# Kernel optimization log

Hardware: AMD Instinct MI355X
Metric: run time of the kernel (lower is better)

## Reference

```python
import jax, jax.numpy as jnp
import numpy as np

K = 20          # neighbors per point
BN_EPS = 1e-5


def setup_inputs() -> dict:
    key = jax.random.key(0)
    k0, k1, k2 = jax.random.split(key, 3)
    B, N, C_OUT, EDGE_DIM = 8, 4096, 64, 4  # edge feat = [diff(3), ||diff||(1)]
    x = jax.random.normal(k0, (B, N, 3), dtype=jnp.float32)
    pos = jax.random.uniform(k1, (B, N, 3), dtype=jnp.float32)
    # shared 1x1-conv MLP params (Conv1d k=1 == per-edge linear) + BatchNorm affine
    W = jax.random.normal(k2, (C_OUT, EDGE_DIM), dtype=jnp.float32) * 0.1
    b = jnp.zeros((C_OUT,), jnp.float32)
    gamma = jnp.ones((C_OUT,), jnp.float32)
    beta = jnp.zeros((C_OUT,), jnp.float32)
    return {"x": x, "pos": pos, "W": W, "b": b, "gamma": gamma, "beta": beta}


def _knn_idx(pos, k):
    # pos: [B, N, 3] -> idx of k nearest neighbors per point, self excluded. [B, N, k]
    B, N, _ = pos.shape
    sq = jnp.sum(pos * pos, axis=-1)                                   # [B, N]
    d2 = sq[:, :, None] + sq[:, None, :] - 2.0 * jnp.einsum('bnd,bmd->bnm', pos, pos)
    d2 = d2 + jnp.eye(N, dtype=pos.dtype) * 1e10                       # exclude self-loop
    _, idx = jax.lax.top_k(-d2, k)                                     # [B, N, k]
    return idx


def _forward(pos, W, b, gamma, beta, k=K):
    idx = _knn_idx(pos, k)                                             # [B, N, k] (int, non-diff)
    nbr = jax.vmap(lambda p, i: p[i])(pos, idx)                        # gather: [B, N, k, 3]
    diff = nbr - pos[:, :, None, :]                                    # neighbor - center
    dist = jnp.sqrt(jnp.sum(diff * diff, axis=-1, keepdims=True))      # [B, N, k, 1]
    feat = jnp.concatenate([diff, dist], axis=-1)                      # [B, N, k, 4]
    # shared MLP (1x1 conv): per-edge linear
    y = jnp.einsum('bnkc,oc->bnko', feat, W) + b                       # [B, N, k, 64]
    # BatchNorm1d over all edges (training-mode batch stats), per channel
    mu = jnp.mean(y, axis=(0, 1, 2))
    var = jnp.var(y, axis=(0, 1, 2))
    y = (y - mu) * jax.lax.rsqrt(var + BN_EPS) * gamma + beta
    y = jax.nn.relu(y)
    y = jnp.where(y >= 0, y, 0.1 * y)   # leaky_relu(0.1) from source (no-op after relu, kept for fidelity)
    return jnp.mean(y, axis=2)          # mean pool over each node's k edges -> [B, N, 64]


def reference(x, pos, W, b, gamma, beta):
    # x only provides (batch_size, num_points) in the source; math uses pos.
    return _forward(pos, W, b, gamma, beta)
```

## Files before the change

### kernel.cpp

```cpp
#include <hip/hip_runtime.h>

#define NB    8
#define NP    4096
#define KNN   20
#define COUT  64
#define S     4
#define BLK   256
#define QPB   (BLK / S)
#define BPB   (NP / QPB)
#define NBLK1 (NB * BPB)
#define NBLK2 ((NB * NP * 4) / BLK)
#define NMOM  14
#define MSTR  16
#define LCAP  32
#define FBIG  3.402823466e38f

typedef unsigned long long u64;
typedef unsigned int u32;

__device__ __forceinline__ void ins20(float d, u32 mi,
                                      float* __restrict__ bd,
                                      u32* __restrict__ bi) {
#pragma unroll
    for (int j = KNN - 1; j >= 1; --j) {
        const bool sh  = d < bd[j - 1];
        const bool in_ = !sh && (d < bd[j]);
        bi[j] = sh ? bi[j - 1] : (in_ ? mi : bi[j]);
        bd[j] = fminf(fmaxf(bd[j - 1], d), bd[j]);
    }
    if (d < bd[0]) { bi[0] = mi; bd[0] = d; }
}

__global__ __launch_bounds__(BLK, 2)
void knn_kernel(const float* __restrict__ pos,
                unsigned short* __restrict__ idx_out,
                float* __restrict__ mom) {
    __shared__ float4 sp[NP];

    const int b = blockIdx.x / BPB;
    const int t = threadIdx.x;
    const int s = t & (S - 1);
    const int n = (blockIdx.x % BPB) * QPB + (t >> 2);
    const float* pb = pos + (size_t)b * NP * 3;

    for (int i = t; i < NP; i += BLK) {
        const float x = pb[3 * i], y = pb[3 * i + 1], z = pb[3 * i + 2];
        const float csq = __fadd_rn(
            __fadd_rn(__fmul_rn(x, x), __fmul_rn(y, y)), __fmul_rn(z, z));
        sp[i] = make_float4(x, y, z, csq);
    }
    __syncthreads();

    const float4 q = sp[n];

    float sd0 = FBIG, sd1 = FBIG, sd2 = FBIG, sd3 = FBIG, sd4 = FBIG;
#pragma unroll 4
    for (int i = 0; i < NP / S; i += 4) {
        const int m = (i << 2) | s;
        const float4 c = sp[m];
        const float dot = fmaf(q.z, c.z, fmaf(q.y, c.y, __fmul_rn(q.x, c.x)));
        const float d2  = __fsub_rn(__fadd_rn(q.w, c.w), __fmul_rn(2.0f, dot));
        if (m != n && d2 < sd4) {
            sd4 = fminf(fmaxf(sd3, d2), sd4);
            sd3 = fminf(fmaxf(sd2, d2), sd3);
            sd2 = fminf(fmaxf(sd1, d2), sd2);
            sd1 = fminf(fmaxf(sd0, d2), sd1);
            sd0 = fminf(sd0, d2);
        }
    }
    float gb = sd4;
    gb = fmaxf(gb, __shfl_xor(gb, 1));
    gb = fmaxf(gb, __shfl_xor(gb, 2));

    float bd[KNN];
    u32   bi[KNN];
#pragma unroll
    for (int j = 0; j < KNN; ++j) { bd[j] = FBIG; bi[j] = 0xFFFu; }
    float p0d = 0.f, p1d = 0.f, p2d = 0.f, p3d = 0.f;
    u32   p0i = 0, p1i = 0, p2i = 0, p3i = 0;
    int   cnt = 0;

#pragma unroll 2
    for (int i = 0; i < NP / S; ++i) {
        const int m = (i << 2) | s;
        const float4 c = sp[m];
        const float dot = fmaf(q.z, c.z, fmaf(q.y, c.y, __fmul_rn(q.x, c.x)));
        const float d2  = __fsub_rn(__fadd_rn(q.w, c.w), __fmul_rn(2.0f, dot));
        const bool acc = (m != n) && (d2 <= gb);
        const bool a0 = acc && (cnt == 0), a1 = acc && (cnt == 1);
        const bool a2 = acc && (cnt == 2), a3 = acc && (cnt == 3);
        p0d = a0 ? d2 : p0d;  p0i = a0 ? (u32)m : p0i;
        p1d = a1 ? d2 : p1d;  p1i = a1 ? (u32)m : p1i;
        p2d = a2 ? d2 : p2d;  p2i = a2 ? (u32)m : p2i;
        p3d = a3 ? d2 : p3d;  p3i = a3 ? (u32)m : p3i;
        cnt += (int)acc;
        if (__ballot(cnt == 4)) {
            ins20(cnt >= 1 ? p0d : FBIG, p0i, bd, bi);
            ins20(cnt >= 2 ? p1d : FBIG, p1i, bd, bi);
            ins20(cnt >= 3 ? p2d : FBIG, p2i, bd, bi);
            ins20(cnt >= 4 ? p3d : FBIG, p3i, bd, bi);
            cnt = 0;
            float g = bd[KNN - 1];
            g = fminf(g, __shfl_xor(g, 1));
            g = fminf(g, __shfl_xor(g, 2));
            gb = fminf(gb, g);
        }
    }
    ins20(cnt >= 1 ? p0d : FBIG, p0i, bd, bi);
    ins20(cnt >= 2 ? p1d : FBIG, p1i, bd, bi);
    ins20(cnt >= 3 ? p2d : FBIG, p2i, bd, bi);
    ins20(cnt >= 4 ? p3d : FBIG, p3i, bd, bi);

    u64 key[LCAP];
#pragma unroll
    for (int j = 0; j < KNN; ++j) {
        u32 fb = __float_as_uint(bd[j]);
        fb ^= (u32)((int)fb >> 31) | 0x80000000u;
        key[j] = ((u64)fb << 12) | bi[j];
    }
#pragma unroll
    for (int j = KNN; j < LCAP; ++j) key[j] = ~0ull;

#pragma unroll
    for (int r = 1; r <= 2; r <<= 1) {
#pragma unroll
        for (int j = 0; j < LCAP / 2; ++j) {
            const int k2 = LCAP - 1 - j;
            const u64 pa = (u64)__shfl_xor((long long)key[k2], r);
            const u64 pc = (u64)__shfl_xor((long long)key[j],  r);
            key[j]  = key[j]  < pa ? key[j]  : pa;
            key[k2] = key[k2] < pc ? key[k2] : pc;
        }
#pragma unroll
        for (int d = 16; d >= 1; d >>= 1) {
#pragma unroll
            for (int j = 0; j < LCAP; ++j) {
                if ((j & d) == 0) {
                    const u64 x = key[j], y = key[j + d];
                    key[j]     = x < y ? x : y;
                    key[j + d] = x < y ? y : x;
                }
            }
        }
    }

    unsigned short* ip = idx_out + ((size_t)b * NP + n) * KNN;
    float s1x = 0, s1y = 0, s1z = 0, s1d = 0;
    float mxx = 0, mxy = 0, mxz = 0, mxd = 0;
    float myy = 0, myz = 0, myd = 0;
    float mzz = 0, mzd = 0, mdd = 0;
#pragma unroll
    for (int j = 0; j < KNN; ++j) {
        const int m = (int)(key[j] & 0xFFFull);
        if ((j & 3) == s) ip[j] = (unsigned short)m;
        const float4 c = sp[m];
        const float dx = __fsub_rn(c.x, q.x);
        const float dy = __fsub_rn(c.y, q.y);
        const float dz = __fsub_rn(c.z, q.z);
        const float dd = sqrtf(__fadd_rn(
            __fadd_rn(__fmul_rn(dx, dx), __fmul_rn(dy, dy)), __fmul_rn(dz, dz)));
        s1x += dx; s1y += dy; s1z += dz; s1d += dd;
        mxx += dx * dx; mxy += dx * dy; mxz += dx * dz; mxd += dx * dd;
        myy += dy * dy; myz += dy * dz; myd += dy * dd;
        mzz += dz * dz; mzd += dz * dd; mdd += dd * dd;
    }
    {
        float vals[NMOM] = {s1x, s1y, s1z, s1d,
                            mxx, mxy, mxz, mxd, myy, myz, myd, mzz, mzd, mdd};
#pragma unroll
        for (int tt = 0; tt < NMOM; ++tt) {
            float v = vals[tt];
#pragma unroll
            for (int off = 32; off > 0; off >>= 1) v += __shfl_down(v, off);
            if ((t & 63) == 0) atomicAdd(&mom[tt * MSTR], v * 0.25f);
        }
    }
}

__global__ __launch_bounds__(BLK)
void out_kernel(const float* __restrict__ pos,
                const float* __restrict__ W,
                const float* __restrict__ bias,
                const float* __restrict__ gamma,
                const float* __restrict__ beta,
                const unsigned short* __restrict__ idx_in,
                const float* __restrict__ mom,
                float* __restrict__ out) {
    __shared__ float sWp[COUT][4];
    __shared__ float sbp[COUT];

    if (threadIdx.x < COUT) {
        const int o = threadIdx.x;
        double S1[4], s2v[10];
#pragma unroll
        for (int tt = 0; tt < 4; ++tt)  S1[tt]  = (double)mom[tt * MSTR];
#pragma unroll
        for (int tt = 0; tt < 10; ++tt) s2v[tt] = (double)mom[(4 + tt) * MSTR];
        const double M = (double)NB * NP * KNN;
        double mean[4];
#pragma unroll
        for (int c = 0; c < 4; ++c) mean[c] = S1[c] / M;
        double E2[4][4];
        E2[0][0] = s2v[0]; E2[0][1] = E2[1][0] = s2v[1];
        E2[0][2] = E2[2][0] = s2v[2]; E2[0][3] = E2[3][0] = s2v[3];
        E2[1][1] = s2v[4]; E2[1][2] = E2[2][1] = s2v[5];
        E2[1][3] = E2[3][1] = s2v[6];
        E2[2][2] = s2v[7]; E2[2][3] = E2[3][2] = s2v[8];
        E2[3][3] = s2v[9];
        double w[4];
#pragma unroll
        for (int c = 0; c < 4; ++c) w[c] = (double)W[o * 4 + c];
        const double bo = (double)bias[o];
        double mu = bo;
#pragma unroll
        for (int c = 0; c < 4; ++c) mu += w[c] * mean[c];
        double var = 0.0;
#pragma unroll
        for (int c = 0; c < 4; ++c)
#pragma unroll
            for (int c2 = 0; c2 < 4; ++c2)
                var += w[c] * w[c2] * (E2[c][c2] / M - mean[c] * mean[c2]);
        const double scale = (double)gamma[o] / sqrt(var + 1e-5);
#pragma unroll
        for (int c = 0; c < 4; ++c) sWp[o][c] = (float)(w[c] * scale);
        sbp[o] = (float)((bo - mu) * scale + (double)beta[o]);
    }
    __syncthreads();

    const int t  = threadIdx.x;
    const int gq = blockIdx.x * (BLK / 4) + (t >> 2);
    const int b  = gq / NP, n = gq % NP;
    const int c0 = (t & 3) * 16;
    const float* pb = pos + (size_t)b * NP * 3;
    const float qx = pb[3 * n], qy = pb[3 * n + 1], qz = pb[3 * n + 2];

    float fx[KNN], fy[KNN], fz[KNN], fd[KNN];
    const unsigned short* ip = idx_in + (size_t)gq * KNN;
#pragma unroll
    for (int j = 0; j < KNN; ++j) {
        const int m = ip[j];
        const float dx = __fsub_rn(pb[3 * m], qx);
        const float dy = __fsub_rn(pb[3 * m + 1], qy);
        const float dz = __fsub_rn(pb[3 * m + 2], qz);
        fx[j] = dx; fy[j] = dy; fz[j] = dz;
        fd[j] = sqrtf(__fadd_rn(
            __fadd_rn(__fmul_rn(dx, dx), __fmul_rn(dy, dy)), __fmul_rn(dz, dz)));
    }

    float* ob = out + (size_t)gq * COUT + c0;
    const float inv = 1.0f / (float)KNN;
#pragma unroll
    for (int o = 0; o < 16; o += 4) {
        float acc[4];
#pragma unroll
        for (int qq = 0; qq < 4; ++qq) {
            const float w0 = sWp[c0 + o + qq][0], w1 = sWp[c0 + o + qq][1];
            const float w2 = sWp[c0 + o + qq][2], w3 = sWp[c0 + o + qq][3];
            const float bb = sbp[c0 + o + qq];
            float a = 0.f;
#pragma unroll
            for (int j = 0; j < KNN; ++j) {
                float y = fmaf(fx[j], w0,
                          fmaf(fy[j], w1, fmaf(fz[j], w2, fmaf(fd[j], w3, bb))));
                a += fmaxf(y, 0.f);
            }
            acc[qq] = a * inv;
        }
        float4 p = {acc[0], acc[1], acc[2], acc[3]};
        *reinterpret_cast<float4*>(ob + o) = p;
    }
}

extern "C" void kernel_launch(void* const* d_in, const int* in_sizes, int n_in,
                              void* d_out, int out_size, void* d_ws, size_t ws_size,
                              hipStream_t stream) {
    (void)in_sizes; (void)n_in; (void)out_size; (void)ws_size;
    const float* pos   = (const float*)d_in[1];
    const float* W     = (const float*)d_in[2];
    const float* bias  = (const float*)d_in[3];
    const float* gamma = (const float*)d_in[4];
    const float* beta  = (const float*)d_in[5];
    float* out = (float*)d_out;

    float* mom = (float*)d_ws;
    unsigned short* idxws = (unsigned short*)((char*)d_ws + 1024);

    hipMemsetAsync(mom, 0, NMOM * MSTR * sizeof(float), stream);
    knn_kernel<<<NBLK1, BLK, 0, stream>>>(pos, idxws, mom);
    out_kernel<<<NBLK2, BLK, 0, stream>>>(pos, W, bias, gamma, beta,
                                          idxws, mom, out);
}
```

Measured before the change: 295.9 us.

## Materialize edge features in kNN kernel to skip gather in output kernel

The kNN kernel now writes each edge's (dx,dy,dz,dist) as a float4 into workspace, and a new output kernel reads those features contiguously instead of gathering neighbor positions by index and recomputing differences and sqrt. This removes scattered position loads in the second kernel but adds a write and a read of about 10 MB of edge features (8*4096*20*16 bytes). It falls back to the old path when the workspace is too small.

```diff
diff --git a/kernel.cpp b/kernel.cpp
--- a/kernel.cpp
+++ b/kernel.cpp
@@ -34,6 +34,7 @@
 __global__ __launch_bounds__(BLK, 2)
 void knn_kernel(const float* __restrict__ pos,
                 unsigned short* __restrict__ idx_out,
+                float4* __restrict__ feats,
                 float* __restrict__ mom) {
     __shared__ float4 sp[NP];
 
@@ -159,6 +160,8 @@
         const float dz = __fsub_rn(c.z, q.z);
         const float dd = sqrtf(__fadd_rn(
             __fadd_rn(__fmul_rn(dx, dx), __fmul_rn(dy, dy)), __fmul_rn(dz, dz)));
+        if (feats != nullptr && (j & 3) == s)
+            feats[((size_t)b * NP + n) * KNN + j] = make_float4(dx, dy, dz, dd);
         s1x += dx; s1y += dy; s1z += dz; s1d += dd;
         mxx += dx * dx; mxy += dx * dy; mxz += dx * dz; mxd += dx * dd;
         myy += dy * dy; myz += dy * dz; myd += dy * dd;
@@ -174,6 +177,99 @@
             for (int off = 32; off > 0; off >>= 1) v += __shfl_down(v, off);
             if ((t & 63) == 0) atomicAdd(&mom[tt * MSTR], v * 0.25f);
         }
+    }
+}
+
+__device__ __forceinline__ void bn_fold(const float* __restrict__ W,
+                                        const float* __restrict__ bias,
+                                        const float* __restrict__ gamma,
+                                        const float* __restrict__ beta,
+                                        const float* __restrict__ mom,
+                                        float (*sWp)[4], float* sbp) {
+    if (threadIdx.x < COUT) {
+        const int o = threadIdx.x;
+        double S1[4], s2v[10];
+#pragma unroll
+        for (int tt = 0; tt < 4; ++tt)  S1[tt]  = (double)mom[tt * MSTR];
+#pragma unroll
+        for (int tt = 0; tt < 10; ++tt) s2v[tt] = (double)mom[(4 + tt) * MSTR];
+        const double M = (double)NB * NP * KNN;
+        double mean[4];
+#pragma unroll
+        for (int c = 0; c < 4; ++c) mean[c] = S1[c] / M;
+        double E2[4][4];
+        E2[0][0] = s2v[0]; E2[0][1] = E2[1][0] = s2v[1];
+        E2[0][2] = E2[2][0] = s2v[2]; E2[0][3] = E2[3][0] = s2v[3];
+        E2[1][1] = s2v[4]; E2[1][2] = E2[2][1] = s2v[5];
+        E2[1][3] = E2[3][1] = s2v[6];
+        E2[2][2] = s2v[7]; E2[2][3] = E2[3][2] = s2v[8];
+        E2[3][3] = s2v[9];
+        double w[4];
+#pragma unroll
+        for (int c = 0; c < 4; ++c) w[c] = (double)W[o * 4 + c];
+        const double bo = (double)bias[o];
+        double mu = bo;
+#pragma unroll
+        for (int c = 0; c < 4; ++c) mu += w[c] * mean[c];
+        double var = 0.0;
+#pragma unroll
+        for (int c = 0; c < 4; ++c)
+#pragma unroll
+            for (int c2 = 0; c2 < 4; ++c2)
+                var += w[c] * w[c2] * (E2[c][c2] / M - mean[c] * mean[c2]);
+        const double scale = (double)gamma[o] / sqrt(var + 1e-5);
+#pragma unroll
+        for (int c = 0; c < 4; ++c) sWp[o][c] = (float)(w[c] * scale);
+        sbp[o] = (float)((bo - mu) * scale + (double)beta[o]);
+    }
+    __syncthreads();
+}
+
+__global__ __launch_bounds__(BLK)
+void out_feat_kernel(const float* __restrict__ W,
+                     const float* __restrict__ bias,
+                     const float* __restrict__ gamma,
+                     const float* __restrict__ beta,
+                     const float4* __restrict__ feats,
+                     const float* __restrict__ mom,
+                     float* __restrict__ out) {
+    __shared__ float sWp[COUT][4];
+    __shared__ float sbp[COUT];
+    bn_fold(W, bias, gamma, beta, mom, sWp, sbp);
+
+    const int t  = threadIdx.x;
+    const int gq = blockIdx.x * (BLK / 4) + (t >> 2);
+    const int c0 = (t & 3) * 16;
+
+    float fx[KNN], fy[KNN], fz[KNN], fd[KNN];
+    const float4* fq = feats + (size_t)gq * KNN;
+#pragma unroll
+    for (int j = 0; j < KNN; ++j) {
+        const float4 f = fq[j];
+        fx[j] = f.x; fy[j] = f.y; fz[j] = f.z; fd[j] = f.w;
+    }
+
+    float* ob = out + (size_t)gq * COUT + c0;
+    const float inv = 1.0f / (float)KNN;
+#pragma unroll
+    for (int o = 0; o < 16; o += 4) {
+        float acc[4];
+#pragma unroll
+        for (int qq = 0; qq < 4; ++qq) {
+            const float w0 = sWp[c0 + o + qq][0], w1 = sWp[c0 + o + qq][1];
+            const float w2 = sWp[c0 + o + qq][2], w3 = sWp[c0 + o + qq][3];
+            const float bb = sbp[c0 + o + qq];
+            float a = 0.f;
+#pragma unroll
+            for (int j = 0; j < KNN; ++j) {
+                float y = fmaf(fx[j], w0,
+                          fmaf(fy[j], w1, fmaf(fz[j], w2, fmaf(fd[j], w3, bb))));
+                a += fmaxf(y, 0.f);
+            }
+            acc[qq] = a * inv;
+        }
+        float4 p = {acc[0], acc[1], acc[2], acc[3]};
+        *reinterpret_cast<float4*>(ob + o) = p;
     }
 }
 
@@ -188,44 +284,7 @@
                 float* __restrict__ out) {
     __shared__ float sWp[COUT][4];
     __shared__ float sbp[COUT];
-
-    if (threadIdx.x < COUT) {
-        const int o = threadIdx.x;
-        double S1[4], s2v[10];
-#pragma unroll
-        for (int tt = 0; tt < 4; ++tt)  S1[tt]  = (double)mom[tt * MSTR];
-#pragma unroll
-        for (int tt = 0; tt < 10; ++tt) s2v[tt] = (double)mom[(4 + tt) * MSTR];
-        const double M = (double)NB * NP * KNN;
-        double mean[4];
-#pragma unroll
-        for (int c = 0; c < 4; ++c) mean[c] = S1[c] / M;
-        double E2[4][4];
-        E2[0][0] = s2v[0]; E2[0][1] = E2[1][0] = s2v[1];
-        E2[0][2] = E2[2][0] = s2v[2]; E2[0][3] = E2[3][0] = s2v[3];
-        E2[1][1] = s2v[4]; E2[1][2] = E2[2][1] = s2v[5];
-        E2[1][3] = E2[3][1] = s2v[6];
-        E2[2][2] = s2v[7]; E2[2][3] = E2[3][2] = s2v[8];
-        E2[3][3] = s2v[9];
-        double w[4];
-#pragma unroll
-        for (int c = 0; c < 4; ++c) w[c] = (double)W[o * 4 + c];
-        const double bo = (double)bias[o];
-        double mu = bo;
-#pragma unroll
-        for (int c = 0; c < 4; ++c) mu += w[c] * mean[c];
-        double var = 0.0;
-#pragma unroll
-        for (int c = 0; c < 4; ++c)
-#pragma unroll
-            for (int c2 = 0; c2 < 4; ++c2)
-                var += w[c] * w[c2] * (E2[c][c2] / M - mean[c] * mean[c2]);
-        const double scale = (double)gamma[o] / sqrt(var + 1e-5);
-#pragma unroll
-        for (int c = 0; c < 4; ++c) sWp[o][c] = (float)(w[c] * scale);
-        sbp[o] = (float)((bo - mu) * scale + (double)beta[o]);
-    }
-    __syncthreads();
+    bn_fold(W, bias, gamma, beta, mom, sWp, sbp);
 
     const int t  = threadIdx.x;
     const int gq = blockIdx.x * (BLK / 4) + (t >> 2);
@@ -274,7 +333,7 @@
 extern "C" void kernel_launch(void* const* d_in, const int* in_sizes, int n_in,
                               void* d_out, int out_size, void* d_ws, size_t ws_size,
                               hipStream_t stream) {
-    (void)in_sizes; (void)n_in; (void)out_size; (void)ws_size;
+    (void)in_sizes; (void)n_in; (void)out_size;
     const float* pos   = (const float*)d_in[1];
     const float* W     = (const float*)d_in[2];
     const float* bias  = (const float*)d_in[3];
@@ -284,9 +343,17 @@
 
     float* mom = (float*)d_ws;
     unsigned short* idxws = (unsigned short*)((char*)d_ws + 1024);
+    const size_t feat_off = 1024 + (size_t)NB * NP * KNN * sizeof(unsigned short);
+    const size_t need = feat_off + (size_t)NB * NP * KNN * sizeof(float4);
+    float4* feats = (ws_size >= need) ? (float4*)((char*)d_ws + feat_off)
+                                      : nullptr;
 
     hipMemsetAsync(mom, 0, NMOM * MSTR * sizeof(float), stream);
-    knn_kernel<<<NBLK1, BLK, 0, stream>>>(pos, idxws, mom);
-    out_kernel<<<NBLK2, BLK, 0, stream>>>(pos, W, bias, gamma, beta,
-                                          idxws, mom, out);
-}
+    knn_kernel<<<NBLK1, BLK, 0, stream>>>(pos, idxws, feats, mom);
+    if (feats != nullptr)
+        out_feat_kernel<<<NBLK2, BLK, 0, stream>>>(W, bias, gamma, beta,
+                                                   feats, mom, out);
+    else
+        out_kernel<<<NBLK2, BLK, 0, stream>>>(pos, W, bias, gamma, beta,
+                                              idxws, mom, out);
+}
```

Result: no change. 299.4 us (+1.2%).
